# Optimization experiments

Hardware: AMD Instinct MI355X
Metric: run time of the kernel (lower is better)

Reference implementation:

```python
import jax, jax.numpy as jnp
import numpy as np

B, S, H = 4, 2048, 16
HID = 2048
Q_LORA = 1536
KV_LORA = 512
D_NOPE, D_ROPE, D_V = 128, 64, 128
D_QK = D_NOPE + D_ROPE  # 192
THETA = 10000.0
EPS = 1e-6


def rms_norm(x, w):
    var = jnp.mean(jnp.square(x), axis=-1, keepdims=True)
    return x * jax.lax.rsqrt(var + EPS) * w


def rotate_half(x):
    x1, x2 = jnp.split(x, 2, axis=-1)
    return jnp.concatenate([-x2, x1], axis=-1)


def apply_rope(x, cos, sin):
    # DeepSeek de-interleaves pairs before the rotate_half formulation
    b, h, s, d = x.shape
    x = x.reshape(b, h, s, d // 2, 2).transpose(0, 1, 2, 4, 3).reshape(b, h, s, d)
    return x * cos + rotate_half(x) * sin


def setup_inputs() -> dict:
    key = jax.random.key(0)
    ks = jax.random.split(key, 8)
    sc = lambda fan_in: 1.0 / np.sqrt(fan_in)
    return {
        "x": jax.random.normal(ks[0], (B, S, HID), jnp.float32),
        "q_a_w": jax.random.normal(ks[1], (Q_LORA, HID), jnp.float32) * sc(HID),
        "q_a_ln_w": jnp.ones((Q_LORA,), jnp.float32),
        "q_b_w": jax.random.normal(ks[2], (H * D_QK, Q_LORA), jnp.float32) * sc(Q_LORA),
        "kv_a_w": jax.random.normal(ks[3], (KV_LORA + D_ROPE, HID), jnp.float32) * sc(HID),
        "kv_a_ln_w": jnp.ones((KV_LORA,), jnp.float32),
        "kv_b_w": jax.random.normal(ks[4], (H * (D_NOPE + D_V), KV_LORA), jnp.float32) * sc(KV_LORA),
        "o_w": jax.random.normal(ks[5], (HID, H * D_V), jnp.float32) * sc(H * D_V),
    }


def reference(x, q_a_w, q_a_ln_w, q_b_w, kv_a_w, kv_a_ln_w, kv_b_w, o_w):
    b, s, _ = x.shape
    # --- Q path: low-rank down-proj -> RMSNorm -> up-proj ---
    q = rms_norm(x @ q_a_w.T, q_a_ln_w) @ q_b_w.T          # [b,s,H*D_QK]
    q = q.reshape(b, s, H, D_QK).transpose(0, 2, 1, 3)      # [b,H,s,D_QK]
    q_nope, q_pe = q[..., :D_NOPE], q[..., D_NOPE:]
    # --- KV path: joint low-rank compression + shared rope key ---
    ckv = x @ kv_a_w.T                                      # [b,s,KV_LORA+D_ROPE]
    c_kv, k_pe = ckv[..., :KV_LORA], ckv[..., KV_LORA:]
    k_pe = k_pe.reshape(b, 1, s, D_ROPE)                    # shared across heads (MQA-style)
    kv = rms_norm(c_kv, kv_a_ln_w) @ kv_b_w.T               # [b,s,H*(D_NOPE+D_V)]
    kv = kv.reshape(b, s, H, D_NOPE + D_V).transpose(0, 2, 1, 3)
    k_nope, v = kv[..., :D_NOPE], kv[..., D_NOPE:]
    # --- decoupled RoPE on the rope sub-dims ---
    inv_freq = 1.0 / (THETA ** (jnp.arange(0, D_ROPE, 2, dtype=jnp.float32) / D_ROPE))
    t = jnp.arange(s, dtype=jnp.float32)
    emb = jnp.concatenate([jnp.outer(t, inv_freq)] * 2, axis=-1)  # [s,D_ROPE]
    cos, sin = jnp.cos(emb)[None, None], jnp.sin(emb)[None, None]
    q_pe = apply_rope(q_pe, cos, sin)
    k_pe = apply_rope(k_pe, cos, sin)
    # --- attention (wrapper's all-True mask => unmasked softmax) ---
    q_full = jnp.concatenate([q_nope, q_pe], axis=-1)                       # [b,H,s,192]
    k_full = jnp.concatenate([k_nope, jnp.broadcast_to(k_pe, (b, H, s, D_ROPE))], axis=-1)
    scale = D_QK ** -0.5
    scores = jnp.einsum('bhqd,bhkd->bhqk', q_full, k_full) * scale
    attn = jax.nn.softmax(scores, axis=-1)
    out = jnp.einsum('bhqk,bhkd->bhqd', attn, v)
    out = out.transpose(0, 2, 1, 3).reshape(b, s, H * D_V)
    return out @ o_w.T
```

## Files before the change

kernel.cpp:

```cpp
#include <hip/hip_runtime.h>
#include <hip/hip_bf16.h>
#include <cstdint>
#include <cstddef>

typedef unsigned short u16;
typedef unsigned int   u32;

typedef __bf16 bf16x8 __attribute__((ext_vector_type(8)));
typedef float  f32x4  __attribute__((ext_vector_type(4)));
typedef float  f32x16 __attribute__((ext_vector_type(16)));
typedef u16    u16x4  __attribute__((ext_vector_type(4)));
typedef u16    u16x8  __attribute__((ext_vector_type(8)));
typedef u32    u32x4  __attribute__((ext_vector_type(4)));

#define DEV static __device__ __forceinline__
#define VMCNT(n) asm volatile("s_waitcnt vmcnt(" #n ")" ::: "memory")
#define LGKM0    asm volatile("s_waitcnt lgkmcnt(0)" ::: "memory")
#define SBARF    do { asm volatile("" ::: "memory"); __builtin_amdgcn_s_barrier(); asm volatile("" ::: "memory"); } while (0)

DEV u16 f2bf(float f){
  union { float f; u32 u; } v; v.f = f;
  u32 r = v.u + 0x7fffu + ((v.u >> 16) & 1u);
  return (u16)(r >> 16);
}
DEV float bf2f(u16 h){
  union { u32 u; float f; } v; v.u = ((u32)h) << 16;
  return v.f;
}
DEV u32 pk2(float a, float b){
  __hip_bfloat16 x = __float2bfloat16(a), y = __float2bfloat16(b);
  return (u32)__builtin_bit_cast(u16, x) | ((u32)__builtin_bit_cast(u16, y) << 16);
}
DEV float fexp2(float x){ float r; asm("v_exp_f32 %0, %1" : "=v"(r) : "v"(x)); return r; }
DEV float mx3(float a, float b, float c){ return fmaxf(fmaxf(a, b), c); }
DEV float tree16(const f32x16& p){
  float a = mx3(p[0],p[1],p[2]),  b = mx3(p[3],p[4],p[5]);
  float c = mx3(p[6],p[7],p[8]),  d = mx3(p[9],p[10],p[11]);
  float e = mx3(p[12],p[13],p[14]);
  return fmaxf(mx3(a,b,c), mx3(d,e,p[15]));
}
DEV void gll16(const void* g, void* l){
  __builtin_amdgcn_global_load_lds(
      (const __attribute__((address_space(1))) u32*)g,
      (__attribute__((address_space(3))) u32*)l, 16, 0, 0);
}

__global__ void k_cvt_all(const float* __restrict__ x,  const float* __restrict__ qaw,
                          const float* __restrict__ kvaw, const float* __restrict__ qbw,
                          const float* __restrict__ kvbw, const float* __restrict__ ow,
                          u16* __restrict__ xb, u16* __restrict__ w1, u16* __restrict__ wqb,
                          u16* __restrict__ wkvb, u16* __restrict__ wo,
                          float* __restrict__ tab){
  const long stride = (long)gridDim.x * blockDim.x;
  for (long i = (long)blockIdx.x * blockDim.x + threadIdx.x; i < 8192000L; i += stride){
    if (i >= 8126464L){
      int idx = (int)(i - 8126464L);
      int s = idx >> 5, p = idx & 31;
      float freq = exp2f(-(float)p * 0.41524101186f);
      float ang = (float)s * freq;
      tab[idx*2]   = cosf(ang);
      tab[idx*2+1] = sinf(ang);
      continue;
    }
    const float* src; u16* dst;
    if (i < 4194304L){ long e = i*4; src = x + e; dst = xb + e; }
    else if (i < 5373952L){
      long e = (i - 4194304L) * 4;
      int row = (int)(e >> 11), col = (int)(e & 2047);
      dst = w1 + e;
      if (row < 1536) src = qaw + (long)row*2048 + col;
      else if (row < 2112) src = kvaw + (long)(row-1536)*2048 + col;
      else { u16x4 z; z[0]=0;z[1]=0;z[2]=0;z[3]=0; *(u16x4*)dst = z; continue; }
    }
    else if (i < 6553600L){
      long e = (i - 5373952L)*4;
      int row = (int)(e / 1536), col = (int)(e - (long)row*1536);
      int dd = row % 192;
      int srow = row;
      if (dd >= 128){
        int j = dd - 128;
        int sdd = (j < 32) ? (128 + 2*j) : (128 + 2*(j - 32) + 1);
        srow = row - dd + sdd;
      }
      src = qbw + (long)srow*1536 + col; dst = wqb + e;
    }
    else if (i < 7077888L){ long e = (i - 6553600L)*4; src = kvbw + e; dst = wkvb + e; }
    else { long e = (i - 7077888L)*4; src = ow + e; dst = wo + e; }
    f32x4 f = *(const f32x4*)src;
    u16x4 o4;
    o4[0]=f2bf(f[0]); o4[1]=f2bf(f[1]); o4[2]=f2bf(f[2]); o4[3]=f2bf(f[3]);
    *(u16x4*)dst = o4;
  }
}

template<int CMODE>
DEV void gemm_body(u16 (*sm)[32768], int bm, int bn,
                   const u16* __restrict__ A, int lda,
                   const u16* __restrict__ B, int ldb,
                   void* __restrict__ Cp, int ldc, int K, int Nlim,
                   u16* __restrict__ kn, u16* __restrict__ vt,
                   const float* __restrict__ tab)
{
  const int tid = threadIdx.x;
  const int l   = tid & 63;
  const int wv  = tid >> 6;
  const int wr  = wv >> 2, wc = wv & 3;
  const int l15 = l & 15, l4 = l >> 4;
  const long M0 = (long)bm * 256, N0 = (long)bn * 256;

  const int c7 = tid & 7;
  const u16* asrc[4]; const u16* bsrc[4];
  int dsta[4], dstb[4];
  #pragma unroll
  for (int s = 0; s < 4; ++s){
    int slot = s*512 + tid;
    int row  = slot >> 3;
    asrc[s] = A + (M0 + row)*lda + ((c7 ^ (row & 7)) << 3);
    bsrc[s] = B + (N0 + row)*ldb + ((c7 ^ (row & 7)) << 3);
    dsta[s] = slot*8;
    dstb[s] = 16384 + slot*8;
  }
  auto stA = [&](int s, int kt, int nb){ gll16(asrc[s] + (long)kt*64, &sm[nb][dsta[s]]); };
  auto stB = [&](int s, int kt, int nb){ gll16(bsrc[s] + (long)kt*64, &sm[nb][dstb[s]]); };

  auto rdA = [&](int buf, int m, int ks) -> bf16x8 {
    int row = wr*128 + m*16 + l15;
    int ch  = ks*4 + l4;
    return *(const bf16x8*)&sm[buf][row*64 + ((ch ^ (row & 7)) << 3)];
  };
  auto rdB = [&](int buf, int n, int ks) -> bf16x8 {
    int row = wc*64 + n*16 + l15;
    int ch  = ks*4 + l4;
    return *(const bf16x8*)&sm[buf][16384 + row*64 + ((ch ^ (row & 7)) << 3)];
  };

  f32x4 acc[8][4];
  #pragma unroll
  for (int m = 0; m < 8; ++m)
    #pragma unroll
    for (int n = 0; n < 4; ++n)
      acc[m][n] = (f32x4)0.0f;

  stB(0,0,0); stB(2,0,0); stB(1,0,0); stB(3,0,0);
  stA(0,0,0); stA(2,0,0); stA(1,0,0); stA(3,0,0);
  VMCNT(2);
  SBARF;

  const int NT = K >> 6;
  for (int t = 0; t < NT; ++t){
    const int cb = t & 1, nb = cb ^ 1;
    const bool PF = (t + 1 < NT);
    bf16x8 bfr[4][2];
    #pragma unroll
    for (int p = 0; p < 4; ++p){
      bf16x8 af[2][2];
      #pragma unroll
      for (int mm = 0; mm < 2; ++mm)
        #pragma unroll
        for (int ks = 0; ks < 2; ++ks)
          af[mm][ks] = rdA(cb, p*2 + mm, ks);
      if (p == 0){
        #pragma unroll
        for (int n = 0; n < 4; ++n)
          #pragma unroll
          for (int ks = 0; ks < 2; ++ks)
            bfr[n][ks] = rdB(cb, n, ks);
        if (PF){ stB(0, t+1, nb); stB(2, t+1, nb); }
      } else if (p == 1){
        if (PF){ stB(1, t+1, nb); stB(3, t+1, nb); }
      } else if (p == 2){
        if (PF){ stA(0, t+1, nb); stA(2, t+1, nb); }
      } else {
        if (PF){ stA(1, t+1, nb); stA(3, t+1, nb); }
      }
      SBARF;
      LGKM0;
      __builtin_amdgcn_s_setprio(1);
      #pragma unroll
      for (int mm = 0; mm < 2; ++mm)
        #pragma unroll
        for (int n = 0; n < 4; ++n)
          #pragma unroll
          for (int ks = 0; ks < 2; ++ks)
            acc[p*2+mm][n] = __builtin_amdgcn_mfma_f32_16x16x32_bf16(af[mm][ks], bfr[n][ks], acc[p*2+mm][n], 0, 0, 0);
      __builtin_amdgcn_s_setprio(0);
      if (p == 1){ if (PF) VMCNT(4); else VMCNT(0); }
      if (p == 3 && PF) VMCNT(2);
      SBARF;
    }
  }

  const long rbase = M0 + wr*128 + l4*4;
  const long cbase = N0 + wc*64 + l15;

  if (CMODE == 3){
    const bool ropeblk = (((N0 + wc*64) % 192) == 128);
    if (ropeblk){
      #pragma unroll
      for (int n = 0; n < 2; ++n){
        const int p = l15 + 16*n;
        #pragma unroll
        for (int m = 0; m < 8; ++m){
          #pragma unroll
          for (int i = 0; i < 4; ++i){
            long r = rbase + m*16 + i;
            const float* cs2 = tab + (((int)(r & 2047))*32 + p)*2;
            float cs = cs2[0], sn = cs2[1];
            float e = acc[m][n][i], o = acc[m][n+2][i];
            ((u16*)Cp)[r * ldc + cbase + n*16]       = f2bf(e*cs - o*sn);
            ((u16*)Cp)[r * ldc + cbase + (n+2)*16]   = f2bf(o*cs + e*sn);
          }
        }
      }
    } else {
      #pragma unroll
      for (int m = 0; m < 8; ++m)
        #pragma unroll
        for (int n = 0; n < 4; ++n)
          #pragma unroll
          for (int i = 0; i < 4; ++i)
            ((u16*)Cp)[(rbase + m*16 + i) * ldc + cbase + n*16] = f2bf(acc[m][n][i]);
    }
    return;
  }

  #pragma unroll
  for (int m = 0; m < 8; ++m){
    #pragma unroll
    for (int n = 0; n < 4; ++n){
      const long c  = cbase + n*16;
      const long r0 = rbase + m*16;
      if (CMODE == 0){
        if (c < Nlim){
          #pragma unroll
          for (int i = 0; i < 4; ++i)
            ((u16*)Cp)[(r0 + i) * ldc + c] = f2bf(acc[m][n][i]);
        }
      } else if (CMODE == 1){
        #pragma unroll
        for (int i = 0; i < 4; ++i)
          ((float*)Cp)[(r0 + i) * ldc + c] = acc[m][n][i];
      } else {
        int h = (int)(c >> 8), rem = (int)(c & 255);
        if (rem < 128){
          #pragma unroll
          for (int i = 0; i < 4; ++i)
            kn[(r0 + i) * 2048 + h*128 + rem] = f2bf(acc[m][n][i]);
        } else {
          int bb = (int)(r0 >> 11), s = (int)(r0 & 2047);
          int kk = s & 63;
          int kkp = (kk & ~12) | ((kk & 4) << 1) | ((kk & 8) >> 1);
          int kt = s >> 6;
          int dfull = rem - 128;
          int bh = bb*16 + h;
          long idx = ((((long)bh*32 + kt)*4 + (dfull>>5))*8 + (kkp>>3))*256
                   + (dfull & 31)*8 + (kkp & 7);
          u16x4 pv;
          #pragma unroll
          for (int i = 0; i < 4; ++i) pv[i] = f2bf(acc[m][n][i]);
          *(u16x4*)&vt[idx] = pv;
        }
      }
    }
  }
}

template<int CMODE>
__global__ __launch_bounds__(512, 1)
void k_gemm8(const u16* __restrict__ A, int lda,
             const u16* __restrict__ B, int ldb,
             void* __restrict__ Cp, int ldc, int K, int Nlim, int gy,
             u16* __restrict__ kn, u16* __restrict__ vt)
{
  __shared__ u16 sm[2][32768];
  const int flat = blockIdx.x;
  const int id2  = (flat & 7) * ((int)gridDim.x >> 3) + (flat >> 3);
  gemm_body<CMODE>(sm, id2 / gy, id2 % gy, A, lda, B, ldb, Cp, ldc, K, Nlim, kn, vt, nullptr);
}

__global__ __launch_bounds__(512, 1)
void k_gemm_qbkvb(const u16* __restrict__ qackv, const u16* __restrict__ wqb,
                  const u16* __restrict__ wkvb, u16* __restrict__ q,
                  u16* __restrict__ kn, u16* __restrict__ vt,
                  const float* __restrict__ tab)
{
  __shared__ u16 sm[2][32768];
  const int flat = blockIdx.x;
  const int grp = flat >> 3, sub = flat & 7;
  if (grp < 48){
    int i = sub*48 + grp;
    gemm_body<3>(sm, i/12, i%12, qackv, 2176, wqb, 1536, q, 3072, 1536, 3072, nullptr, nullptr, tab);
  } else {
    int i = sub*64 + (grp - 48);
    gemm_body<2>(sm, i/16, i%16, qackv + 1536, 2176, wkvb, 512, nullptr, 0, 512, 4096, kn, vt, nullptr);
  }
}

__global__ __launch_bounds__(256)
void k_normrope(u16* __restrict__ qackv, const float* __restrict__ qln,
                const float* __restrict__ kvln){
  const int tok = blockIdx.x;
  const int tid = threadIdx.x;
  u16* row = qackv + (long)tok * 2176;
  __shared__ float red[8];

  float v[6]; float ss = 0.f;
  #pragma unroll
  for (int i = 0; i < 6; ++i){
    int c = tid + i*256;
    v[i] = bf2f(row[c]);
    ss += v[i]*v[i];
  }
  #pragma unroll
  for (int m = 32; m >= 1; m >>= 1) ss += __shfl_xor(ss, m);
  if ((tid & 63) == 0) red[tid >> 6] = ss;
  __syncthreads();
  float tot = red[0] + red[1] + red[2] + red[3];
  float r1 = rsqrtf(tot * (1.0f/1536.0f) + 1e-6f);
  #pragma unroll
  for (int i = 0; i < 6; ++i){
    int c = tid + i*256;
    row[c] = f2bf(v[i] * r1 * qln[c]);
  }

  float u0 = bf2f(row[1536 + tid]);
  float u1 = bf2f(row[1536 + 256 + tid]);
  float s2 = u0*u0 + u1*u1;
  #pragma unroll
  for (int m = 32; m >= 1; m >>= 1) s2 += __shfl_xor(s2, m);
  if ((tid & 63) == 0) red[4 + (tid >> 6)] = s2;
  __syncthreads();
  float tot2 = red[4] + red[5] + red[6] + red[7];
  float r2 = rsqrtf(tot2 * (1.0f/512.0f) + 1e-6f);
  row[1536 + tid]       = f2bf(u0 * r2 * kvln[tid]);
  row[1536 + 256 + tid] = f2bf(u1 * r2 * kvln[256 + tid]);

  if (tid < 32){
    int p = tid;
    u32 pair = *(const u32*)(row + 2048 + 2*p);
    float e = bf2f((u16)(pair & 0xffff));
    float o = bf2f((u16)(pair >> 16));
    int s = tok & 2047;
    float freq = exp2f(-(float)p * 0.41524101186f);
    float ang = (float)s * freq;
    float cs = cosf(ang), sn = sinf(ang);
    row[2048 + p]      = f2bf(e*cs - o*sn);
    row[2048 + 32 + p] = f2bf(o*cs + e*sn);
  }
}

__global__ __launch_bounds__(512)
void k_attn11(const u16* __restrict__ Q, const u16* __restrict__ KN,
              const u16* __restrict__ CKV, const u16* __restrict__ VT,
              u16* __restrict__ O)
{
  __shared__ u16 sK[2][64*192];

  const int tid = threadIdx.x;
  const int l   = tid & 63;
  const int w   = tid >> 6;
  const int l31 = l & 31;
  const int hi  = l >> 5;
  const int swz = l31 & 7;
  const int flat = blockIdx.x;
  const int qb  = flat >> 6;
  const int bh  = ((flat & 7) << 3) | ((flat >> 3) & 7);
  const int b   = bh >> 4, h = bh & 15;
  const long tokbase = (long)b << 11;

  bf16x8 qf[12];
  {
    const u16* qptr = Q + (tokbase + qb*256 + w*32 + l31)*3072 + h*192 + hi*8;
    #pragma unroll
    for (int s = 0; s < 12; ++s)
      qf[s] = *(const bf16x8*)(qptr + s*16);
  }

  const u16* ksrc[3]; int kstep[3]; int kdst[3];
  #pragma unroll
  for (int i = 0; i < 3; ++i){
    int ch = tid + i*512;
    int row = ch / 24;
    int cc  = ch - row*24;
    int sc  = cc ^ (row & 7);
    if (sc < 16){ ksrc[i] = KN  + (tokbase + row)*2048 + h*128 + sc*8;       kstep[i] = 64*2048; }
    else        { ksrc[i] = CKV + (tokbase + row)*2176 + 2048 + (sc-16)*8;   kstep[i] = 64*2176; }
    kdst[i] = ch*8;
  }
  auto STAGE = [&](int kt, int nb){
    #pragma unroll
    for (int i = 0; i < 3; ++i) gll16(ksrc[i] + (long)kt*kstep[i], &sK[nb][kdst[i]]);
  };

  const u16* vbase = VT + (long)bh*(32*8192) + hi*256 + l31*8;

  f32x16 oacc[4];
  #pragma unroll
  for (int i = 0; i < 4; ++i) oacc[i] = (f32x16)0.0f;
  float mrun = -1e30f, lrun = 0.f;
  const float scale2 = (float)(0.07216878364870323 * 1.4426950408889634);

  STAGE(0, 0);
  __syncthreads();

  for (int kt = 0; kt < 32; ++kt){
    const int cur = kt & 1;
    if (kt < 31) STAGE(kt + 1, cur ^ 1);

    const char* kb = (const char*)&sK[cur][0];
    const u16*  vp = vbase + (long)kt*8192;

    f32x16 p0 = (f32x16)0.0f, p1 = (f32x16)0.0f;
    __builtin_amdgcn_s_setprio(1);
    #pragma unroll
    for (int s = 0; s < 12; ++s){
      const int co = ((2*s + hi) ^ swz) << 4;
      bf16x8 k0 = *(const bf16x8*)(kb + l31*384 + co);
      bf16x8 k1 = *(const bf16x8*)(kb + (32 + l31)*384 + co);
      p0 = __builtin_amdgcn_mfma_f32_32x32x16_bf16(k0, qf[s], p0, 0, 0, 0);
      p1 = __builtin_amdgcn_mfma_f32_32x32x16_bf16(k1, qf[s], p1, 0, 0, 0);
    }
    __builtin_amdgcn_s_setprio(0);

    bf16x8 vA0 = *(const bf16x8*)(vp + 0);
    bf16x8 vA1 = *(const bf16x8*)(vp + 2048);
    bf16x8 vA2 = *(const bf16x8*)(vp + 4096);
    bf16x8 vA3 = *(const bf16x8*)(vp + 6144);
    bf16x8 vB0 = *(const bf16x8*)(vp + 512);
    bf16x8 vB1 = *(const bf16x8*)(vp + 2560);
    bf16x8 vB2 = *(const bf16x8*)(vp + 4608);
    bf16x8 vB3 = *(const bf16x8*)(vp + 6656);

    float rm = fmaxf(tree16(p0), tree16(p1));
    rm = fmaxf(rm, __shfl_xor(rm, 32));
    const float om = rm * scale2;
    if (!__all(om <= mrun + 8.0f)){
      float mn = fmaxf(mrun, om);
      float corr = fexp2(mrun - mn);
      mrun = mn;
      lrun *= corr;
      #pragma unroll
      for (int d = 0; d < 4; ++d)
        #pragma unroll
        for (int r = 0; r < 16; ++r) oacc[d][r] *= corr;
    }
    float ls = 0.f;
    #pragma unroll
    for (int r = 0; r < 16; ++r){ p0[r] = fexp2(__builtin_fmaf(p0[r], scale2, -mrun)); ls += p0[r]; }
    #pragma unroll
    for (int r = 0; r < 16; ++r){ p1[r] = fexp2(__builtin_fmaf(p1[r], scale2, -mrun)); ls += p1[r]; }
    lrun += ls + __shfl_xor(ls, 32);

    bf16x8 pa[4];
    #pragma unroll
    for (int ks = 0; ks < 4; ++ks){
      const f32x16 ps = (ks < 2) ? p0 : p1;
      const int rb = (ks & 1) * 8;
      u32x4 aw;
      aw[0] = pk2(ps[rb+0], ps[rb+1]);
      aw[1] = pk2(ps[rb+2], ps[rb+3]);
      aw[2] = pk2(ps[rb+4], ps[rb+5]);
      aw[3] = pk2(ps[rb+6], ps[rb+7]);
      pa[ks] = __builtin_bit_cast(bf16x8, aw);
    }
    __builtin_amdgcn_s_setprio(1);
    bf16x8 vC0 = *(const bf16x8*)(vp + 1024);
    bf16x8 vC1 = *(const bf16x8*)(vp + 3072);
    bf16x8 vC2 = *(const bf16x8*)(vp + 5120);
    bf16x8 vC3 = *(const bf16x8*)(vp + 7168);
    oacc[0] = __builtin_amdgcn_mfma_f32_32x32x16_bf16(vA0, pa[0], oacc[0], 0, 0, 0);
    oacc[1] = __builtin_amdgcn_mfma_f32_32x32x16_bf16(vA1, pa[0], oacc[1], 0, 0, 0);
    oacc[2] = __builtin_amdgcn_mfma_f32_32x32x16_bf16(vA2, pa[0], oacc[2], 0, 0, 0);
    oacc[3] = __builtin_amdgcn_mfma_f32_32x32x16_bf16(vA3, pa[0], oacc[3], 0, 0, 0);
    bf16x8 vD0 = *(const bf16x8*)(vp + 1536);
    bf16x8 vD1 = *(const bf16x8*)(vp + 3584);
    bf16x8 vD2 = *(const bf16x8*)(vp + 5632);
    bf16x8 vD3 = *(const bf16x8*)(vp + 7680);
    oacc[0] = __builtin_amdgcn_mfma_f32_32x32x16_bf16(vB0, pa[1], oacc[0], 0, 0, 0);
    oacc[1] = __builtin_amdgcn_mfma_f32_32x32x16_bf16(vB1, pa[1], oacc[1], 0, 0, 0);
    oacc[2] = __builtin_amdgcn_mfma_f32_32x32x16_bf16(vB2, pa[1], oacc[2], 0, 0, 0);
    oacc[3] = __builtin_amdgcn_mfma_f32_32x32x16_bf16(vB3, pa[1], oacc[3], 0, 0, 0);
    oacc[0] = __builtin_amdgcn_mfma_f32_32x32x16_bf16(vC0, pa[2], oacc[0], 0, 0, 0);
    oacc[1] = __builtin_amdgcn_mfma_f32_32x32x16_bf16(vC1, pa[2], oacc[1], 0, 0, 0);
    oacc[2] = __builtin_amdgcn_mfma_f32_32x32x16_bf16(vC2, pa[2], oacc[2], 0, 0, 0);
    oacc[3] = __builtin_amdgcn_mfma_f32_32x32x16_bf16(vC3, pa[2], oacc[3], 0, 0, 0);
    oacc[0] = __builtin_amdgcn_mfma_f32_32x32x16_bf16(vD0, pa[3], oacc[0], 0, 0, 0);
    oacc[1] = __builtin_amdgcn_mfma_f32_32x32x16_bf16(vD1, pa[3], oacc[1], 0, 0, 0);
    oacc[2] = __builtin_amdgcn_mfma_f32_32x32x16_bf16(vD2, pa[3], oacc[2], 0, 0, 0);
    oacc[3] = __builtin_amdgcn_mfma_f32_32x32x16_bf16(vD3, pa[3], oacc[3], 0, 0, 0);
    __builtin_amdgcn_s_setprio(0);

    __syncthreads();
  }

  const float inv = 1.0f / lrun;
  u16* optr = O + (tokbase + qb*256 + w*32 + l31)*2048 + h*128;
  #pragma unroll
  for (int d = 0; d < 4; ++d){
    #pragma unroll
    for (int t = 0; t < 4; ++t){
      u16x4 ov;
      #pragma unroll
      for (int j = 0; j < 4; ++j) ov[j] = f2bf(oacc[d][4*t + j] * inv);
      *(u16x4*)(optr + d*32 + 8*t + 4*hi) = ov;
    }
  }
}

extern "C" void kernel_launch(void* const* d_in, const int* in_sizes, int n_in,
                              void* d_out, int out_size, void* d_ws, size_t ws_size,
                              hipStream_t stream)
{
  const float* x    = (const float*)d_in[0];
  const float* qaw  = (const float*)d_in[1];
  const float* qln  = (const float*)d_in[2];
  const float* qbw  = (const float*)d_in[3];
  const float* kvaw = (const float*)d_in[4];
  const float* kvln = (const float*)d_in[5];
  const float* kvbw = (const float*)d_in[6];
  const float* ow   = (const float*)d_in[7];

  char* ws = (char*)d_ws;
  size_t off = 0;
  auto alloc = [&](size_t bytes) -> void* {
    void* p = ws + off;
    off += (bytes + 255) & ~(size_t)255;
    return p;
  };
  u16* xb    = (u16*)alloc(8192UL*2048*2);
  u16* w1    = (u16*)alloc(2304UL*2048*2);
  u16* wqb   = (u16*)alloc(3072UL*1536*2);
  u16* wkvb  = (u16*)alloc(4096UL*512*2);
  u16* wo    = (u16*)alloc(2048UL*2048*2);
  u16* qackv = (u16*)alloc(8192UL*2176*2);
  u16* q     = (u16*)alloc(8192UL*3072*2);
  u16* kn    = (u16*)alloc(8192UL*2048*2);
  u16* vt    = (u16*)alloc(8192UL*2048*2);
  float* tab = (float*)alloc(2048UL*32*2*4);
  u16* ao    = xb;

  k_cvt_all<<<dim3(2048), dim3(256), 0, stream>>>(x, qaw, kvaw, qbw, kvbw, ow,
                                                  xb, w1, wqb, wkvb, wo, tab);
  k_gemm8<0><<<dim3(288), dim3(512), 0, stream>>>(xb, 2048, w1, 2048,
                                                  qackv, 2176, 2048, 2176, 9, nullptr, nullptr);
  k_normrope<<<dim3(8192), dim3(256), 0, stream>>>(qackv, qln, kvln);
  k_gemm_qbkvb<<<dim3(896), dim3(512), 0, stream>>>(qackv, wqb, wkvb, q, kn, vt, tab);
  k_attn11<<<dim3(512), dim3(512), 0, stream>>>(q, kn, qackv, vt, ao);
  k_gemm8<1><<<dim3(256), dim3(512), 0, stream>>>(ao, 2048, wo, 2048,
                                                  d_out, 2048, 2048, 2048, 8, nullptr, nullptr);
}
```

Baseline: 527.9 us.

## Software-pipeline attention loop: overlap next QK^T with previous softmax and PV

Restructures the flash-attention inner loop so the QK^T MFMAs for tile kt are issued alongside the softmax and PV update for tile kt-1, with a prologue and epilogue and a loop unrolled by two that ping-pongs score registers. The goal is to hide the exp/max/pack latency of softmax behind matrix-core work instead of running them back to back. It keeps two sets of score accumulators live, which raises register pressure and could cost occupancy or cause spills.

```diff
diff --git a/kernel.cpp b/kernel.cpp
--- a/kernel.cpp
+++ b/kernel.cpp
@@ -350,7 +350,7 @@
 }
 
 __global__ __launch_bounds__(512)
-void k_attn11(const u16* __restrict__ Q, const u16* __restrict__ KN,
+void k_attn15(const u16* __restrict__ Q, const u16* __restrict__ KN,
               const u16* __restrict__ CKV, const u16* __restrict__ VT,
               u16* __restrict__ O)
 {
@@ -400,28 +400,57 @@
   float mrun = -1e30f, lrun = 0.f;
   const float scale2 = (float)(0.07216878364870323 * 1.4426950408889634);
 
-  STAGE(0, 0);
-  __syncthreads();
-
-  for (int kt = 0; kt < 32; ++kt){
-    const int cur = kt & 1;
-    if (kt < 31) STAGE(kt + 1, cur ^ 1);
-
-    const char* kb = (const char*)&sK[cur][0];
-    const u16*  vp = vbase + (long)kt*8192;
-
-    f32x16 p0 = (f32x16)0.0f, p1 = (f32x16)0.0f;
+  auto QK = [&](f32x16& P0, f32x16& P1, const char* kb){
+    P0 = (f32x16)0.0f; P1 = (f32x16)0.0f;
     __builtin_amdgcn_s_setprio(1);
     #pragma unroll
     for (int s = 0; s < 12; ++s){
       const int co = ((2*s + hi) ^ swz) << 4;
       bf16x8 k0 = *(const bf16x8*)(kb + l31*384 + co);
       bf16x8 k1 = *(const bf16x8*)(kb + (32 + l31)*384 + co);
-      p0 = __builtin_amdgcn_mfma_f32_32x32x16_bf16(k0, qf[s], p0, 0, 0, 0);
-      p1 = __builtin_amdgcn_mfma_f32_32x32x16_bf16(k1, qf[s], p1, 0, 0, 0);
+      P0 = __builtin_amdgcn_mfma_f32_32x32x16_bf16(k0, qf[s], P0, 0, 0, 0);
+      P1 = __builtin_amdgcn_mfma_f32_32x32x16_bf16(k1, qf[s], P1, 0, 0, 0);
     }
     __builtin_amdgcn_s_setprio(0);
-
+  };
+
+  auto FINISH = [&](f32x16& P0, f32x16& P1, bf16x8* pa){
+    float rm = fmaxf(tree16(P0), tree16(P1));
+    rm = fmaxf(rm, __shfl_xor(rm, 32));
+    const float om = rm * scale2;
+    if (!__all(om <= mrun + 8.0f)){
+      float mn = fmaxf(mrun, om);
+      float corr = fexp2(mrun - mn);
+      mrun = mn;
+      lrun *= corr;
+      #pragma unroll
+      for (int d = 0; d < 4; ++d)
+        #pragma unroll
+        for (int r = 0; r < 16; ++r) oacc[d][r] *= corr;
+    }
+    float ls = 0.f;
+    #pragma unroll
+    for (int r = 0; r < 16; ++r){ P0[r] = fexp2(__builtin_fmaf(P0[r], scale2, -mrun)); ls += P0[r]; }
+    #pragma unroll
+    for (int r = 0; r < 16; ++r){ P1[r] = fexp2(__builtin_fmaf(P1[r], scale2, -mrun)); ls += P1[r]; }
+    lrun += ls + __shfl_xor(ls, 32);
+    #pragma unroll
+    for (int ks = 0; ks < 4; ++ks){
+      const f32x16 ps = (ks < 2) ? P0 : P1;
+      const int rb = (ks & 1) * 8;
+      u32x4 aw;
+      aw[0] = pk2(ps[rb+0], ps[rb+1]);
+      aw[1] = pk2(ps[rb+2], ps[rb+3]);
+      aw[2] = pk2(ps[rb+4], ps[rb+5]);
+      aw[3] = pk2(ps[rb+6], ps[rb+7]);
+      pa[ks] = __builtin_bit_cast(bf16x8, aw);
+    }
+  };
+
+  auto ITER = [&](int curkt, const char* kbcur, int nb,
+                  f32x16& Pc0, f32x16& Pc1, f32x16& Pp0, f32x16& Pp1){
+    if (curkt < 31) STAGE(curkt + 1, nb);
+    const u16* vp = vbase + (long)(curkt - 1) * 8192;
     bf16x8 vA0 = *(const bf16x8*)(vp + 0);
     bf16x8 vA1 = *(const bf16x8*)(vp + 2048);
     bf16x8 vA2 = *(const bf16x8*)(vp + 4096);
@@ -431,38 +460,11 @@
     bf16x8 vB2 = *(const bf16x8*)(vp + 4608);
     bf16x8 vB3 = *(const bf16x8*)(vp + 6656);
 
-    float rm = fmaxf(tree16(p0), tree16(p1));
-    rm = fmaxf(rm, __shfl_xor(rm, 32));
-    const float om = rm * scale2;
-    if (!__all(om <= mrun + 8.0f)){
-      float mn = fmaxf(mrun, om);
-      float corr = fexp2(mrun - mn);
-      mrun = mn;
-      lrun *= corr;
-      #pragma unroll
-      for (int d = 0; d < 4; ++d)
-        #pragma unroll
-        for (int r = 0; r < 16; ++r) oacc[d][r] *= corr;
-    }
-    float ls = 0.f;
-    #pragma unroll
-    for (int r = 0; r < 16; ++r){ p0[r] = fexp2(__builtin_fmaf(p0[r], scale2, -mrun)); ls += p0[r]; }
-    #pragma unroll
-    for (int r = 0; r < 16; ++r){ p1[r] = fexp2(__builtin_fmaf(p1[r], scale2, -mrun)); ls += p1[r]; }
-    lrun += ls + __shfl_xor(ls, 32);
+    QK(Pc0, Pc1, kbcur);
 
     bf16x8 pa[4];
-    #pragma unroll
-    for (int ks = 0; ks < 4; ++ks){
-      const f32x16 ps = (ks < 2) ? p0 : p1;
-      const int rb = (ks & 1) * 8;
-      u32x4 aw;
-      aw[0] = pk2(ps[rb+0], ps[rb+1]);
-      aw[1] = pk2(ps[rb+2], ps[rb+3]);
-      aw[2] = pk2(ps[rb+4], ps[rb+5]);
-      aw[3] = pk2(ps[rb+6], ps[rb+7]);
-      pa[ks] = __builtin_bit_cast(bf16x8, aw);
-    }
+    FINISH(Pp0, Pp1, pa);
+
     __builtin_amdgcn_s_setprio(1);
     bf16x8 vC0 = *(const bf16x8*)(vp + 1024);
     bf16x8 vC1 = *(const bf16x8*)(vp + 3072);
@@ -491,6 +493,39 @@
     __builtin_amdgcn_s_setprio(0);
 
     __syncthreads();
+  };
+
+  const char* kb0 = (const char*)&sK[0][0];
+  const char* kb1 = (const char*)&sK[1][0];
+
+  f32x16 pA0, pA1, pB0, pB1;
+
+  STAGE(0, 0);
+  __syncthreads();
+  STAGE(1, 1);
+  QK(pA0, pA1, kb0);
+  __syncthreads();
+
+  for (int t = 0; t < 15; ++t){
+    ITER(2*t + 1, kb1, 0, pB0, pB1, pA0, pA1);
+    ITER(2*t + 2, kb0, 1, pA0, pA1, pB0, pB1);
+  }
+  ITER(31, kb1, 0, pB0, pB1, pA0, pA1);
+
+  {
+    const u16* vp = vbase + 31L*8192;
+    bf16x8 pa[4];
+    FINISH(pB0, pB1, pa);
+    __builtin_amdgcn_s_setprio(1);
+    #pragma unroll
+    for (int ks = 0; ks < 4; ++ks){
+      #pragma unroll
+      for (int d = 0; d < 4; ++d){
+        bf16x8 vf = *(const bf16x8*)(vp + d*2048 + ks*512);
+        oacc[d] = __builtin_amdgcn_mfma_f32_32x32x16_bf16(vf, pa[ks], oacc[d], 0, 0, 0);
+      }
+    }
+    __builtin_amdgcn_s_setprio(0);
   }
 
   const float inv = 1.0f / lrun;
@@ -545,7 +580,7 @@
                                                   qackv, 2176, 2048, 2176, 9, nullptr, nullptr);
   k_normrope<<<dim3(8192), dim3(256), 0, stream>>>(qackv, qln, kvln);
   k_gemm_qbkvb<<<dim3(896), dim3(512), 0, stream>>>(qackv, wqb, wkvb, q, kn, vt, tab);
-  k_attn11<<<dim3(512), dim3(512), 0, stream>>>(q, kn, qackv, vt, ao);
+  k_attn15<<<dim3(512), dim3(512), 0, stream>>>(q, kn, qackv, vt, ao);
   k_gemm8<1><<<dim3(256), dim3(512), 0, stream>>>(ao, 2048, wo, 2048,
                                                   d_out, 2048, 2048, 2048, 8, nullptr, nullptr);
 }
```

Result: slower. 577.1 us (+9.3%).

## Split k_pe projection into dedicated MFMA kernel with fused RoPE epilogue

Applied to the files above, without the earlier changes.

The main down-projection GEMM shrinks from 9 to 8 column tiles so it covers only the q_a and c_kv columns, which are exactly 2048 wide. The previous ninth tile was mostly zero padding for the 64 rope columns. A new small kernel computes the 64 k_pe columns with 16x16x32 MFMAs from de-interleaved weight rows and applies RoPE in registers using the precomputed cos/sin table. The RoPE step and its transcendentals are removed from k_normrope. The trade-off is an extra launch and a low-occupancy 64-thread kernel that rereads all of x from global memory without LDS reuse.

```diff
diff --git a/kernel.cpp b/kernel.cpp
--- a/kernel.cpp
+++ b/kernel.cpp
@@ -69,7 +69,12 @@
       int row = (int)(e >> 11), col = (int)(e & 2047);
       dst = w1 + e;
       if (row < 1536) src = qaw + (long)row*2048 + col;
-      else if (row < 2112) src = kvaw + (long)(row-1536)*2048 + col;
+      else if (row < 2048) src = kvaw + (long)(row-1536)*2048 + col;
+      else if (row < 2112){
+        int j = row - 2048;
+        int sj = (j < 32) ? (2*j) : (2*(j-32)+1);
+        src = kvaw + (long)(512 + sj)*2048 + col;
+      }
       else { u16x4 z; z[0]=0;z[1]=0;z[2]=0;z[3]=0; *(u16x4*)dst = z; continue; }
     }
     else if (i < 6553600L){
@@ -296,6 +301,54 @@
   }
 }
 
+__global__ __launch_bounds__(64)
+void k_kpe(const u16* __restrict__ xb, const u16* __restrict__ w1,
+           u16* __restrict__ qackv, const float* __restrict__ tab)
+{
+  const int l = threadIdx.x;
+  const int l15 = l & 15, l4 = l >> 4;
+  const long M0 = (long)blockIdx.x * 16;
+
+  f32x4 acc[4];
+  #pragma unroll
+  for (int n = 0; n < 4; ++n) acc[n] = (f32x4)0.0f;
+
+  const u16* aptr = xb + (M0 + l15)*2048 + l4*8;
+  const u16* bptr = w1 + (2048 + l15)*2048 + l4*8;
+
+  #pragma unroll 2
+  for (int kt = 0; kt < 32; ++kt){
+    bf16x8 a[2], b[4][2];
+    #pragma unroll
+    for (int ks = 0; ks < 2; ++ks)
+      a[ks] = *(const bf16x8*)(aptr + kt*64 + ks*32);
+    #pragma unroll
+    for (int n = 0; n < 4; ++n)
+      #pragma unroll
+      for (int ks = 0; ks < 2; ++ks)
+        b[n][ks] = *(const bf16x8*)(bptr + (long)n*16*2048 + kt*64 + ks*32);
+    #pragma unroll
+    for (int n = 0; n < 4; ++n)
+      #pragma unroll
+      for (int ks = 0; ks < 2; ++ks)
+        acc[n] = __builtin_amdgcn_mfma_f32_16x16x32_bf16(a[ks], b[n][ks], acc[n], 0, 0, 0);
+  }
+
+  #pragma unroll
+  for (int n = 0; n < 2; ++n){
+    const int p = l15 + 16*n;
+    #pragma unroll
+    for (int i = 0; i < 4; ++i){
+      long r = M0 + l4*4 + i;
+      const float* cs2 = tab + (((int)(r & 2047))*32 + p)*2;
+      float cs = cs2[0], sn = cs2[1];
+      float e = acc[n][i], o = acc[n+2][i];
+      qackv[r*2176 + 2048 + p]      = f2bf(e*cs - o*sn);
+      qackv[r*2176 + 2048 + 32 + p] = f2bf(o*cs + e*sn);
+    }
+  }
+}
+
 __global__ __launch_bounds__(256)
 void k_normrope(u16* __restrict__ qackv, const float* __restrict__ qln,
                 const float* __restrict__ kvln){
@@ -334,19 +387,6 @@
   float r2 = rsqrtf(tot2 * (1.0f/512.0f) + 1e-6f);
   row[1536 + tid]       = f2bf(u0 * r2 * kvln[tid]);
   row[1536 + 256 + tid] = f2bf(u1 * r2 * kvln[256 + tid]);
-
-  if (tid < 32){
-    int p = tid;
-    u32 pair = *(const u32*)(row + 2048 + 2*p);
-    float e = bf2f((u16)(pair & 0xffff));
-    float o = bf2f((u16)(pair >> 16));
-    int s = tok & 2047;
-    float freq = exp2f(-(float)p * 0.41524101186f);
-    float ang = (float)s * freq;
-    float cs = cosf(ang), sn = sinf(ang);
-    row[2048 + p]      = f2bf(e*cs - o*sn);
-    row[2048 + 32 + p] = f2bf(o*cs + e*sn);
-  }
 }
 
 __global__ __launch_bounds__(512)
@@ -541,8 +581,9 @@
 
   k_cvt_all<<<dim3(2048), dim3(256), 0, stream>>>(x, qaw, kvaw, qbw, kvbw, ow,
                                                   xb, w1, wqb, wkvb, wo, tab);
-  k_gemm8<0><<<dim3(288), dim3(512), 0, stream>>>(xb, 2048, w1, 2048,
-                                                  qackv, 2176, 2048, 2176, 9, nullptr, nullptr);
+  k_gemm8<0><<<dim3(256), dim3(512), 0, stream>>>(xb, 2048, w1, 2048,
+                                                  qackv, 2176, 2048, 2176, 8, nullptr, nullptr);
+  k_kpe<<<dim3(512), dim3(64), 0, stream>>>(xb, w1, qackv, tab);
   k_normrope<<<dim3(8192), dim3(256), 0, stream>>>(qackv, qln, kvln);
   k_gemm_qbkvb<<<dim3(896), dim3(512), 0, stream>>>(qackv, wqb, wkvb, q, kn, vt, tab);
   k_attn11<<<dim3(512), dim3(512), 0, stream>>>(q, kn, qackv, vt, ao);
```

Result: faster. 503.8 us (median of 2 runs) (-4.6%).
